# Optimization experiments

Hardware: AMD Instinct MI355X
Metric: run time of the kernel (lower is better)

The kernel has to match this reference:

```python
import jax, jax.numpy as jnp
import numpy as np

NUCLEIC_ACID_CUTOFF = 30.0
OTHER_CUTOFF = 15.0


def _cdist(x):
    # x: [b, n, 3] -> pairwise euclidean distances [b, n, n]
    sq = jnp.sum(x * x, axis=-1)  # [b, n]
    d2 = sq[:, :, None] + sq[:, None, :] - 2.0 * jnp.einsum('bid,bjd->bij', x, x)
    d2 = jnp.maximum(d2, 0.0)
    # safe sqrt (zero diagonal would produce nan grads otherwise)
    safe = jnp.where(d2 > 0.0, d2, 1.0)
    return jnp.where(d2 > 0.0, jnp.sqrt(safe), 0.0)


def setup_inputs() -> dict:
    key = jax.random.key(0)
    k1, k2, k3, k4, k5 = jax.random.split(key, 5)
    b, n = 2, 4096
    # scale ~10 Angstrom spread so distances straddle the 15/30 cutoffs
    true_coords = jax.random.normal(k1, (b, n, 3), dtype=jnp.float32) * 10.0
    pred_coords = true_coords + jax.random.normal(k2, (b, n, 3), dtype=jnp.float32) * 1.5
    is_dna = jax.random.bernoulli(k3, 0.15, (b, n))
    is_rna = jax.random.bernoulli(k4, 0.15, (b, n))
    coords_mask = jax.random.bernoulli(k5, 0.95, (b, n))
    return {
        'pred_coords': pred_coords,
        'true_coords': true_coords,
        'is_dna': is_dna,
        'is_rna': is_rna,
        'coords_mask': coords_mask,
    }


def reference(pred_coords, true_coords, is_dna, is_rna, coords_mask):
    n = pred_coords.shape[1]
    pred_dists = _cdist(pred_coords)  # [b, n, n]
    true_dists = _cdist(true_coords)  # [b, n, n]
    dist_diff = jnp.abs(true_dists - pred_dists)
    eps = (
        jax.nn.sigmoid(0.5 - dist_diff)
        + jax.nn.sigmoid(1.0 - dist_diff)
        + jax.nn.sigmoid(2.0 - dist_diff)
        + jax.nn.sigmoid(4.0 - dist_diff)
    ) / 4.0

    is_nucleotide = is_dna | is_rna  # [b, n]
    is_nucleotide_pair = is_nucleotide[:, :, None] & is_nucleotide[:, None, :]
    inclusion_radius = jnp.where(
        is_nucleotide_pair,
        true_dists < NUCLEIC_ACID_CUTOFF,
        true_dists < OTHER_CUTOFF,
    )
    not_eye = ~jnp.eye(n, dtype=bool)[None, :, :]
    mask = inclusion_radius & not_eye
    mask = mask & (coords_mask[:, :, None] & coords_mask[:, None, :])

    maskf = mask.astype(eps.dtype)
    lddt_sum = jnp.sum(eps * maskf, axis=(-1, -2))  # [b]
    lddt_count = jnp.sum(maskf, axis=(-1, -2))  # [b]
    lddt = lddt_sum / jnp.maximum(lddt_count, 1.0)
    return 1.0 - jnp.mean(lddt)
```

## Files before the change

kernel.cpp:

```cpp
#include <hip/hip_runtime.h>
#include <hip/hip_bf16.h>


#define NRES 4096
#define NBATCH 2
#define TI 8
#define NTILE 9

#define CUT15 21.6404256133f
#define CUT30 43.2808512267f

#define S1 66.35420923f
#define S2 678.60880385f
#define S3 2039.58217570f
#define S4 1808.04241445f
#define QP1 16.58855231f
#define QP2 339.30440193f
#define QP3 1529.68663177f
#define QP4 1808.04241445f

#define LOG2E 1.44269504089f

__global__ void pack_kernel(const float* __restrict__ pred,
                            const float* __restrict__ truec,
                            const int* __restrict__ dna,
                            const int* __restrict__ rna,
                            const int* __restrict__ cm,
                            float4* __restrict__ tp,
                            float4* __restrict__ pp)
{
    int idx = blockIdx.x * 256 + threadIdx.x;
    if (idx >= NRES * NBATCH) return;
    float nuc = ((dna[idx] | rna[idx]) != 0) ? 1.0f : 0.0f;
    float cmf = (cm[idx] != 0) ? 1.0f : 0.0f;
    tp[idx] = make_float4(truec[3*idx+0]*LOG2E, truec[3*idx+1]*LOG2E, truec[3*idx+2]*LOG2E, nuc);
    pp[idx] = make_float4(pred[3*idx+0]*LOG2E,  pred[3*idx+1]*LOG2E,  pred[3*idx+2]*LOG2E,  cmf);
}

#define PAIR_LOOP(MODE)                                                     \
    _Pragma("unroll")                                                       \
    for (int r = 0; r < TI; ++r) {                                          \
        float dx = tix[r] - t4.x, dy = tiy[r] - t4.y, dz = tiz[r] - t4.z;   \
        float dt = __builtin_amdgcn_sqrtf(dx*dx + dy*dy + dz*dz);           \
        float ex = pix[r] - p4.x, ey = piy[r] - p4.y, ez = piz[r] - p4.z;   \
        float dp = __builtin_amdgcn_sqrtf(ex*ex + ey*ey + ez*ez);           \
        float cutoff = nucj ? cHi[r] : cLo[r];                              \
        float mf = (dt < cutoff) ? wj : 0.0f;                               \
        if (MODE == 1) mf = (o >= r + 1) ? mf : 0.0f;                       \
        if (MODE == 2) { int d = o - r;                                     \
            mf = (d <= 2048) ? mf : 0.0f;                                   \
            mf = (d == 2048) ? 0.5f * mf : mf; }                            \
        float t = __builtin_amdgcn_exp2f(-fabsf(dt - dp));                  \
        float Q  = 1.0f + t*(S1 + t*(S2 + t*(S3 + t*S4)));                  \
        float Qp = QP1 + t*(QP2 + t*(QP3 + t*QP4));                         \
        float rq = __builtin_amdgcn_rcpf(Q);                                \
        s += mf * ((t * Qp) * rq);                                          \
        c += mf;                                                            \
    }

__launch_bounds__(256, 4)
__global__ void lddt_main(const float4* __restrict__ tp,
                          const float4* __restrict__ pp,
                          float* __restrict__ acc)
{
    const int b    = blockIdx.y;
    const int i0   = blockIdx.x * TI;
    const int base = b * NRES;
    const int tid  = threadIdx.x;

    float tix[TI], tiy[TI], tiz[TI];
    float pix[TI], piy[TI], piz[TI];
    float cHi[TI], cLo[TI];
    #pragma unroll
    for (int r = 0; r < TI; ++r) {
        float4 t4 = tp[base + i0 + r];
        float4 p4 = pp[base + i0 + r];
        tix[r] = t4.x; tiy[r] = t4.y; tiz[r] = t4.z;
        pix[r] = p4.x; piy[r] = p4.y; piz[r] = p4.z;
        bool cmi  = (p4.w != 0.0f);
        bool nuci = (t4.w != 0.0f);
        cHi[r] = cmi ? (nuci ? CUT30 : CUT15) : -1.0f;
        cLo[r] = cmi ? CUT15 : -1.0f;
    }

    float s = 0.0f, c = 0.0f;

    float4 t4 = tp[base + ((i0 + tid) & (NRES - 1))];
    float4 p4 = pp[base + ((i0 + tid) & (NRES - 1))];

    #pragma unroll 1
    for (int tl = 0; tl < NTILE; ++tl) {
        const int on = (tl == NTILE - 1) ? tid : (tl + 1) * 256 + tid;
        const int jn = (i0 + on) & (NRES - 1);
        float4 t4n = tp[base + jn];
        float4 p4n = pp[base + jn];

        const float wj   = p4.w;
        const bool  nucj = (t4.w != 0.0f);
        const int   o    = tl * 256 + tid;

        if (tl == 0)            { PAIR_LOOP(1) }
        else if (tl == NTILE-1) { PAIR_LOOP(2) }
        else                    { PAIR_LOOP(0) }

        t4 = t4n; p4 = p4n;
    }

    #pragma unroll
    for (int off = 32; off > 0; off >>= 1) {
        s += __shfl_down(s, off, 64);
        c += __shfl_down(c, off, 64);
    }

    __shared__ float red_s[4];
    __shared__ float red_c[4];
    const int wid  = tid >> 6;
    const int lane = tid & 63;
    if (lane == 0) { red_s[wid] = s; red_c[wid] = c; }
    __syncthreads();

    if (tid == 0) {
        float ts = red_s[0] + red_s[1] + red_s[2] + red_s[3];
        float tc = red_c[0] + red_c[1] + red_c[2] + red_c[3];
        atomicAdd(&acc[b], ts);
        atomicAdd(&acc[NBATCH + b], tc);
    }
}

__global__ void lddt_final(const float* __restrict__ acc, float* __restrict__ out)
{
    float l0 = acc[0] / fmaxf(acc[2], 0.5f);
    float l1 = acc[1] / fmaxf(acc[3], 0.5f);
    out[0] = 1.0f - 0.5f * (l0 + l1);
}

extern "C" void kernel_launch(void* const* d_in, const int* in_sizes, int n_in,
                              void* d_out, int out_size, void* d_ws, size_t ws_size,
                              hipStream_t stream) {
    const float* pred  = (const float*)d_in[0];
    const float* truec = (const float*)d_in[1];
    const int*   dna   = (const int*)d_in[2];
    const int*   rna   = (const int*)d_in[3];
    const int*   cmask = (const int*)d_in[4];
    float* out = (float*)d_out;

    char* ws = (char*)d_ws;
    float*  acc = (float*)ws;
    float4* tp  = (float4*)(ws + 1024);
    float4* pp  = (float4*)(ws + 1024 + NBATCH*NRES*16);

    (void)hipMemsetAsync(acc, 0, 4 * sizeof(float), stream);

    pack_kernel<<<(NRES*NBATCH + 255)/256, 256, 0, stream>>>(pred, truec, dna, rna, cmask, tp, pp);

    dim3 grid(NRES / TI, NBATCH);
    lddt_main<<<grid, 256, 0, stream>>>(tp, pp, acc);

    lddt_final<<<1, 1, 0, stream>>>(acc, out);
}
```

Before: 46.87 us.

## Split offset tiles across two blocks and fuse final reduction via last-block atomic

Result: slower. 128.1 us (+173.3%).

```diff
diff --git a/kernel.cpp b/kernel.cpp
--- a/kernel.cpp
+++ b/kernel.cpp
@@ -6,6 +6,8 @@
 #define NBATCH 2
 #define TI 8
 #define NTILE 9
+#define OSPLIT 5
+#define NBLOCKS 2048
 
 #define CUT15 21.6404256133f
 #define CUT30 43.2808512267f
@@ -58,15 +60,21 @@
         c += mf;                                                            \
     }
 
-__launch_bounds__(256, 4)
+__launch_bounds__(256, 8)
 __global__ void lddt_main(const float4* __restrict__ tp,
                           const float4* __restrict__ pp,
-                          float* __restrict__ acc)
+                          float* __restrict__ acc,
+                          unsigned int* __restrict__ done,
+                          float* __restrict__ out)
 {
-    const int b    = blockIdx.y;
+    const int b    = blockIdx.z;
+    const int osel = blockIdx.y;
     const int i0   = blockIdx.x * TI;
     const int base = b * NRES;
     const int tid  = threadIdx.x;
+
+    const int ob = osel ? OSPLIT : 0;
+    const int oe = osel ? NTILE  : OSPLIT;
 
     float tix[TI], tiy[TI], tiz[TI];
     float pix[TI], piy[TI], piz[TI];
@@ -85,12 +93,12 @@
 
     float s = 0.0f, c = 0.0f;
 
-    float4 t4 = tp[base + ((i0 + tid) & (NRES - 1))];
-    float4 p4 = pp[base + ((i0 + tid) & (NRES - 1))];
+    float4 t4 = tp[base + ((i0 + ob * 256 + tid) & (NRES - 1))];
+    float4 p4 = pp[base + ((i0 + ob * 256 + tid) & (NRES - 1))];
 
     #pragma unroll 1
-    for (int tl = 0; tl < NTILE; ++tl) {
-        const int on = (tl == NTILE - 1) ? tid : (tl + 1) * 256 + tid;
+    for (int tl = ob; tl < oe; ++tl) {
+        const int on = ((tl + 1 < oe) ? tl + 1 : ob) * 256 + tid;
         const int jn = (i0 + on) & (NRES - 1);
         float4 t4n = tp[base + jn];
         float4 p4n = pp[base + jn];
@@ -124,14 +132,18 @@
         float tc = red_c[0] + red_c[1] + red_c[2] + red_c[3];
         atomicAdd(&acc[b], ts);
         atomicAdd(&acc[NBATCH + b], tc);
+        __threadfence();
+        unsigned int old = atomicAdd(done, 1u);
+        if (old == NBLOCKS - 1u) {
+            float a0 = __hip_atomic_load(&acc[0], __ATOMIC_ACQUIRE, __HIP_MEMORY_SCOPE_AGENT);
+            float a1 = __hip_atomic_load(&acc[1], __ATOMIC_ACQUIRE, __HIP_MEMORY_SCOPE_AGENT);
+            float c0 = __hip_atomic_load(&acc[2], __ATOMIC_ACQUIRE, __HIP_MEMORY_SCOPE_AGENT);
+            float c1 = __hip_atomic_load(&acc[3], __ATOMIC_ACQUIRE, __HIP_MEMORY_SCOPE_AGENT);
+            float l0 = a0 / fmaxf(c0, 0.5f);
+            float l1 = a1 / fmaxf(c1, 0.5f);
+            out[0] = 1.0f - 0.5f * (l0 + l1);
+        }
     }
-}
-
-__global__ void lddt_final(const float* __restrict__ acc, float* __restrict__ out)
-{
-    float l0 = acc[0] / fmaxf(acc[2], 0.5f);
-    float l1 = acc[1] / fmaxf(acc[3], 0.5f);
-    out[0] = 1.0f - 0.5f * (l0 + l1);
 }
 
 extern "C" void kernel_launch(void* const* d_in, const int* in_sizes, int n_in,
@@ -145,16 +157,15 @@
     float* out = (float*)d_out;
 
     char* ws = (char*)d_ws;
-    float*  acc = (float*)ws;
-    float4* tp  = (float4*)(ws + 1024);
-    float4* pp  = (float4*)(ws + 1024 + NBATCH*NRES*16);
+    float*        acc  = (float*)ws;
+    unsigned int* done = (unsigned int*)(ws + 64);
+    float4* tp = (float4*)(ws + 1024);
+    float4* pp = (float4*)(ws + 1024 + NBATCH*NRES*16);
 
-    (void)hipMemsetAsync(acc, 0, 4 * sizeof(float), stream);
+    (void)hipMemsetAsync(ws, 0, 128, stream);
 
     pack_kernel<<<(NRES*NBATCH + 255)/256, 256, 0, stream>>>(pred, truec, dna, rna, cmask, tp, pp);
 
-    dim3 grid(NRES / TI, NBATCH);
-    lddt_main<<<grid, 256, 0, stream>>>(tp, pp, acc);
-
-    lddt_final<<<1, 1, 0, stream>>>(acc, out);
+    dim3 grid(NRES / TI, 2, NBATCH);
+    lddt_main<<<grid, 256, 0, stream>>>(tp, pp, acc, done, out);
 }
```
